# Kernel optimization log

Measured on AMD Instinct MI355X. Metric: run time of the kernel, lower is better.

## Reference

```python
import jax, jax.numpy as jnp
import numpy as np

NH, NL, NPNT = 8, 4, 4          # heads, levels, points
NQ, BS, NK, D, DFFN = 100, 8, 18, 256, 1024
SPATIAL = np.array([[92, 92], [46, 46], [23, 23], [12, 12]], np.int32)
LEN_MEM = int((SPATIAL[:, 0] * SPATIAL[:, 1]).sum())  # 11253


def _layernorm(x, g, b):
    m = x.mean(-1, keepdims=True)
    v = ((x - m) ** 2).mean(-1, keepdims=True)
    return (x - m) / jnp.sqrt(v + 1e-5) * g + b


def _mha(xq, xk, xv, in_w, in_b, out_w, out_b):
    # torch nn.MultiheadAttention semantics, inputs (S, B, D)
    S, B, d = xq.shape
    dh = d // NH
    wq, wk, wv = jnp.split(in_w, 3, axis=0)
    bq, bk, bv = jnp.split(in_b, 3, axis=0)
    def proj(x, w, b):
        return (x @ w.T + b).reshape(x.shape[0], B, NH, dh).transpose(1, 2, 0, 3)
    q = proj(xq, wq, bq) * (1.0 / np.sqrt(dh))
    k = proj(xk, wk, bk)
    v = proj(xv, wv, bv)
    att = jax.nn.softmax(jnp.einsum('bhqd,bhkd->bhqk', q, k), axis=-1)
    o = jnp.einsum('bhqk,bhkd->bhqd', att, v).transpose(2, 0, 1, 3).reshape(S, B, d)
    return o @ out_w.T + out_b


def _bilinear(v_l, loc):
    # v_l: (bs,H,W,NH,dh); loc: (bs,Lq,NH,P,2) normalized [0,1]
    # matches F.grid_sample(align_corners=False, padding_mode='zeros')
    bs, H, W, nh, dh = v_l.shape
    x = loc[..., 0] * W - 0.5
    y = loc[..., 1] * H - 0.5
    x0 = jnp.floor(x); y0 = jnp.floor(y)
    lx = x - x0; ly = y - y0
    b_idx = jnp.arange(bs)[:, None, None, None]
    h_idx = jnp.arange(nh)[None, None, :, None]
    def corner(xa, ya, w):
        valid = (xa >= 0) & (xa < W) & (ya >= 0) & (ya < H)
        xi = jnp.clip(xa, 0, W - 1).astype(jnp.int32)
        yi = jnp.clip(ya, 0, H - 1).astype(jnp.int32)
        return v_l[b_idx, yi, xi, h_idx] * (w * valid)[..., None]
    return (corner(x0, y0, (1 - lx) * (1 - ly)) + corner(x0 + 1, y0, lx * (1 - ly))
            + corner(x0, y0 + 1, (1 - lx) * ly) + corner(x0 + 1, y0 + 1, lx * ly))


def _msda(q, rp, mem, pad_mask, ss, off_w, off_b, aw_w, aw_b, val_w, val_b, outp_w, outp_b):
    bs, Lq, d = q.shape
    dh = d // NH
    value = mem @ val_w.T + val_b
    value = jnp.where(pad_mask[..., None], 0.0, value).reshape(bs, -1, NH, dh)
    off = (q @ off_w.T + off_b).reshape(bs, Lq, NH, NL, NPNT, 2)
    aw = jax.nn.softmax((q @ aw_w.T + aw_b).reshape(bs, Lq, NH, NL * NPNT), -1)
    aw = aw.reshape(bs, Lq, NH, NL, NPNT)
    wh = jnp.asarray(ss[:, ::-1].copy(), jnp.float32)  # offset normalizer (W, H)
    loc = rp[:, :, None, :, None, :] + off / wh[None, None, None, :, None, :]
    out = jnp.zeros((bs, Lq, NH, dh), q.dtype)
    start = 0
    for l in range(NL):
        H, W = int(ss[l, 0]), int(ss[l, 1])
        v_l = value[:, start:start + H * W].reshape(bs, H, W, NH, dh)
        start += H * W
        samp = _bilinear(v_l, loc[:, :, :, l])          # (bs,Lq,NH,P,dh)
        out = out + (samp * aw[:, :, :, l, :, None]).sum(3)
    return out.reshape(bs, Lq, d) @ outp_w.T + outp_b


def _forward(tgt_pose, pos, ref_points, memory, w_in_w, w_in_b, w_out_w, w_out_b,
             a_in_w, a_in_b, a_out_w, a_out_b, off_w, off_b, aw_w, aw_b,
             val_w, val_b, outp_w, outp_b, wn_g, wn_b, an_g, an_b,
             n1_g, n1_b, n2_g, n2_b, l1_w, l1_b, l2_w, l2_b,
             spatial_shapes, level_start_index, padding_mask):
    ss = np.asarray(jax.device_get(spatial_shapes))
    nq, bs, nk, d = tgt_pose.shape
    # within-group self-attn over the nk keypoint tokens.
    # NOTE: with_pos_embed mutates tgt_pose in place in the torch code, so
    # q = k = v = tgt + pos and the residual also uses tgt + pos (faithful).
    t = tgt_pose + pos
    x = t.reshape(nq * bs, nk, d).transpose(1, 0, 2)   # (nk, nq*bs, d)
    a1 = _mha(x, x, x, w_in_w, w_in_b, w_out_w, w_out_b)
    t = _layernorm(t + a1.transpose(1, 0, 2).reshape(nq, bs, nk, d), wn_g, wn_b)
    # across-group self-attn over the nq groups
    x2 = t.reshape(nq, bs * nk, d)
    a2 = _mha(x2, x2, x2, a_in_w, a_in_b, a_out_w, a_out_b)
    t = _layernorm(t + a2.reshape(nq, bs, nk, d), an_g, an_b)
    # MSDeformAttn cross-attention (in-place pos add again, faithful)
    t = t + pos
    q = t.transpose(1, 0, 2, 3).reshape(bs, nq * nk, d)
    rp = jnp.swapaxes(ref_points, 0, 1)                # (bs, nq*nk, NL, 2)
    mem = jnp.swapaxes(memory, 0, 1)                   # (bs, LEN_MEM, d)
    c = _msda(q, rp, mem, padding_mask, ss, off_w, off_b, aw_w, aw_b,
              val_w, val_b, outp_w, outp_b)
    c = c.reshape(bs, nq, nk, d).transpose(1, 0, 2, 3)
    t = _layernorm(t + c, n1_g, n1_b)
    # FFN (dropout is identity in eval)
    h = jax.nn.relu(t @ l1_w.T + l1_b)
    return _layernorm(t + (h @ l2_w.T + l2_b), n2_g, n2_b)


def setup_inputs() -> dict:
    key = jax.random.key(0)
    ks = jax.random.split(key, 16)
    p = lambda k, shape: jax.random.normal(k, shape, jnp.float32) * 0.02
    lsi = np.concatenate([[0], np.cumsum(SPATIAL[:, 0] * SPATIAL[:, 1])[:-1]]).astype(np.int32)
    return {
        'tgt_pose': jax.random.normal(ks[0], (NQ, BS, NK, D), jnp.float32),
        'pos': jax.random.normal(ks[1], (NQ, BS, NK, D), jnp.float32),
        'ref_points': jax.random.uniform(ks[2], (NQ * NK, BS, NL, 2), jnp.float32),
        'memory': jax.random.normal(ks[3], (LEN_MEM, BS, D), jnp.float32),
        'w_in_w': p(ks[4], (3 * D, D)), 'w_in_b': jnp.zeros((3 * D,)),
        'w_out_w': p(ks[5], (D, D)), 'w_out_b': jnp.zeros((D,)),
        'a_in_w': p(ks[6], (3 * D, D)), 'a_in_b': jnp.zeros((3 * D,)),
        'a_out_w': p(ks[7], (D, D)), 'a_out_b': jnp.zeros((D,)),
        'off_w': p(ks[8], (NH * NL * NPNT * 2, D)),
        'off_b': jax.random.uniform(ks[9], (NH * NL * NPNT * 2,), jnp.float32, -2.0, 2.0),
        'aw_w': p(ks[10], (NH * NL * NPNT, D)), 'aw_b': jnp.zeros((NH * NL * NPNT,)),
        'val_w': p(ks[11], (D, D)), 'val_b': jnp.zeros((D,)),
        'outp_w': p(ks[12], (D, D)), 'outp_b': jnp.zeros((D,)),
        'wn_g': jnp.ones((D,)), 'wn_b': jnp.zeros((D,)),
        'an_g': jnp.ones((D,)), 'an_b': jnp.zeros((D,)),
        'n1_g': jnp.ones((D,)), 'n1_b': jnp.zeros((D,)),
        'n2_g': jnp.ones((D,)), 'n2_b': jnp.zeros((D,)),
        'l1_w': p(ks[13], (DFFN, D)), 'l1_b': jnp.zeros((DFFN,)),
        'l2_w': p(ks[14], (D, DFFN)), 'l2_b': jnp.zeros((D,)),
        'spatial_shapes': jnp.asarray(SPATIAL),
        'level_start_index': jnp.asarray(lsi),
        'padding_mask': jnp.zeros((BS, LEN_MEM), bool),
    }


def reference(tgt_pose, pos, ref_points, memory, w_in_w, w_in_b, w_out_w, w_out_b,
              a_in_w, a_in_b, a_out_w, a_out_b, off_w, off_b, aw_w, aw_b,
              val_w, val_b, outp_w, outp_b, wn_g, wn_b, an_g, an_b,
              n1_g, n1_b, n2_g, n2_b, l1_w, l1_b, l2_w, l2_b,
              spatial_shapes, level_start_index, padding_mask):
    return _forward(tgt_pose, pos, ref_points, memory, w_in_w, w_in_b, w_out_w, w_out_b,
                    a_in_w, a_in_b, a_out_w, a_out_b, off_w, off_b, aw_w, aw_b,
                    val_w, val_b, outp_w, outp_b, wn_g, wn_b, an_g, an_b,
                    n1_g, n1_b, n2_g, n2_b, l1_w, l1_b, l2_w, l2_b,
                    spatial_shapes, level_start_index, padding_mask)
```

## Files before the change

kernel.cpp:

```cpp
#include <hip/hip_runtime.h>
#include <math.h>

#define NH_ 8
#define D_ 256
#define NK_ 18
#define NQ_ 100
#define BS_ 8
#define LQ_ 1800
#define LEN_MEM_ 11253
#define NTOK_ 14400

typedef short bf16x8 __attribute__((ext_vector_type(8)));
typedef float f32x4 __attribute__((ext_vector_type(4)));
typedef unsigned short ushort;

__device__ inline ushort f2bf(float f) {
    unsigned int u = __builtin_bit_cast(unsigned int, f);
    unsigned int r = (u + 0x7fffu + ((u >> 16) & 1u)) >> 16;
    return (ushort)r;
}
__device__ inline float bf2f_hi(unsigned int u) {
    unsigned int i = u & 0xffff0000u;
    return __builtin_bit_cast(float, i);
}
__device__ inline float bf2f_lo(unsigned int u) {
    unsigned int i = u << 16;
    return __builtin_bit_cast(float, i);
}
__device__ inline int packbf2(float a, float b) {
    return (int)f2bf(a) | ((int)f2bf(b) << 16);
}

__global__ __launch_bounds__(256)
void wcvt_kernel(const float* s0, const float* s1, const float* s2, const float* s3,
                 const float* s4, const float* s5, const float* s6, const float* s7,
                 const float* s8, const float* s9, ushort* dst) {
    const int sizes[10] = {196608,65536,196608,65536,65536,32768,65536,65536,262144,262144};
    const int offs[10]  = {0,196608,262144,458752,524288,589824,622592,688128,753664,1015808};
    int ti = blockIdx.y;
    const float* s;
    switch (ti) {
        case 0: s = s0; break; case 1: s = s1; break; case 2: s = s2; break;
        case 3: s = s3; break; case 4: s = s4; break; case 5: s = s5; break;
        case 6: s = s6; break; case 7: s = s7; break; case 8: s = s8; break;
        default: s = s9; break;
    }
    int n = sizes[ti];
    int i = (blockIdx.x * 256 + threadIdx.x) * 8;
    if (i >= n) return;
    ushort* d = dst + offs[ti] + i;
    float4 f0 = *(const float4*)(s + i);
    float4 f1 = *(const float4*)(s + i + 4);
    int4 val;
    val.x = packbf2(f0.x, f0.y);
    val.y = packbf2(f0.z, f0.w);
    val.z = packbf2(f1.x, f1.y);
    val.w = packbf2(f1.z, f1.w);
    *(int4*)d = val;
}

__global__ __launch_bounds__(256)
void addcvt_kernel(const float* __restrict__ a, const float* __restrict__ b,
                   float* __restrict__ c, ushort* __restrict__ cbf, int n4) {
    int i = blockIdx.x * blockDim.x + threadIdx.x;
    if (i >= n4) return;
    float4 av = ((const float4*)a)[i];
    float4 bv = ((const float4*)b)[i];
    float4 cv;
    cv.x = av.x + bv.x; cv.y = av.y + bv.y; cv.z = av.z + bv.z; cv.w = av.w + bv.w;
    ((float4*)c)[i] = cv;
    uint2 p;
    p.x = (unsigned int)packbf2(cv.x, cv.y);
    p.y = (unsigned int)packbf2(cv.z, cv.w);
    *(uint2*)(cbf + (size_t)i * 4) = p;
}

template<int MODE, bool RELU, bool A_F32, bool OUT_BF16, int BN, int WAVES, int R>
__device__ __forceinline__
void gemmw_body(int bx, int by, const void* __restrict__ Av, const ushort* __restrict__ W,
                const float* __restrict__ bias, void* __restrict__ Cv,
                int M, int N, const unsigned char* __restrict__ mask, ushort* Ws) {
    constexpr int K = 256;
    constexpr int NT = BN / 16;
    const int tid = threadIdx.x;
    const int m0 = bx * (WAVES * 16 * R);
    const int n0 = by * BN;

    for (int c = tid; c < 32 * BN; c += WAVES * 64) {
        int kc = c & 31, n = c >> 5;
        int dst = kc * BN + (n ^ (kc & 7));
        *(int4*)(Ws + dst * 8) = *(const int4*)(W + (long)(n0 + n) * K + kc * 8);
    }
    __syncthreads();

    const int wv = tid >> 6, lane = tid & 63, fr = lane & 15, hi = lane >> 4;
    const int wm0 = m0 + wv * (16 * R);
    long arow[R];
#pragma unroll
    for (int r = 0; r < R; ++r) {
        int gr = wm0 + r * 16 + fr;
        if (gr > M - 1) gr = M - 1;
        if (MODE == 2) {
            int b = gr / LQ_; int lq = gr - b * LQ_;
            int q = lq / NK_; int kk = lq - q * NK_;
            arow[r] = (long)q * (BS_ * NK_) + b * NK_ + kk;
        } else {
            arow[r] = gr;
        }
    }

    f32x4 acc[R][NT];
#pragma unroll
    for (int r = 0; r < R; ++r)
#pragma unroll
        for (int t = 0; t < NT; ++t) acc[r][t] = f32x4{0.f, 0.f, 0.f, 0.f};

    if (A_F32) {
        const float* ap[R];
        float4 p0[R], p1[R];
#pragma unroll
        for (int r = 0; r < R; ++r) {
            ap[r] = (const float*)Av + arow[r] * (long)K + hi * 8;
            p0[r] = *(const float4*)ap[r];
            p1[r] = *(const float4*)(ap[r] + 4);
        }
#pragma unroll
        for (int ks = 0; ks < 8; ++ks) {
            bf16x8 cur[R];
#pragma unroll
            for (int r = 0; r < R; ++r) {
                int4 v;
                v.x = packbf2(p0[r].x, p0[r].y); v.y = packbf2(p0[r].z, p0[r].w);
                v.z = packbf2(p1[r].x, p1[r].y); v.w = packbf2(p1[r].z, p1[r].w);
                cur[r] = __builtin_bit_cast(bf16x8, v);
                if (ks < 7) {
                    p0[r] = *(const float4*)(ap[r] + (ks + 1) * 32);
                    p1[r] = *(const float4*)(ap[r] + (ks + 1) * 32 + 4);
                }
            }
            const int kc = ks * 4 + hi;
            const ushort* wb = Ws + ((kc * BN) + (fr ^ (kc & 7))) * 8;
#pragma unroll
            for (int t = 0; t < NT; ++t) {
                bf16x8 wf = *(const bf16x8*)(wb + t * 128);
#pragma unroll
                for (int r = 0; r < R; ++r)
                    acc[r][t] = __builtin_amdgcn_mfma_f32_16x16x32_bf16(cur[r], wf, acc[r][t], 0, 0, 0);
            }
        }
    } else {
        const ushort* ap[R];
        bf16x8 afrag[R];
#pragma unroll
        for (int r = 0; r < R; ++r) {
            ap[r] = (const ushort*)Av + arow[r] * (long)K + hi * 8;
            afrag[r] = *(const bf16x8*)ap[r];
        }
#pragma unroll
        for (int ks = 0; ks < 8; ++ks) {
            bf16x8 cur[R];
#pragma unroll
            for (int r = 0; r < R; ++r) {
                cur[r] = afrag[r];
                if (ks < 7) afrag[r] = *(const bf16x8*)(ap[r] + (ks + 1) * 32);
            }
            const int kc = ks * 4 + hi;
            const ushort* wb = Ws + ((kc * BN) + (fr ^ (kc & 7))) * 8;
#pragma unroll
            for (int t = 0; t < NT; ++t) {
                bf16x8 wf = *(const bf16x8*)(wb + t * 128);
#pragma unroll
                for (int r = 0; r < R; ++r)
                    acc[r][t] = __builtin_amdgcn_mfma_f32_16x16x32_bf16(cur[r], wf, acc[r][t], 0, 0, 0);
            }
        }
    }

#pragma unroll
    for (int r = 0; r < R; ++r) {
#pragma unroll
        for (int rr = 0; rr < 4; ++rr) {
            int gm = wm0 + r * 16 + hi * 4 + rr;
            if (gm >= M) continue;
            long orow = gm;
            bool zero = false;
            if (MODE == 1) {
                if (mask && mask[(size_t)(gm & 7) * LEN_MEM_ + (gm >> 3)]) zero = true;
            } else if (MODE == 3) {
                int b = gm / LQ_; int lq = gm - b * LQ_;
                int q = lq / NK_; int kk = lq - q * NK_;
                orow = (long)q * (BS_ * NK_) + b * NK_ + kk;
            }
#pragma unroll
            for (int t = 0; t < NT; ++t) {
                int gn = n0 + t * 16 + fr;
                float v = acc[r][t][rr] + bias[gn];
                if (RELU) v = fmaxf(v, 0.f);
                if (zero) v = 0.f;
                if (OUT_BF16) ((ushort*)Cv)[orow * (long)N + gn] = f2bf(v);
                else ((float*)Cv)[orow * (long)N + gn] = v;
            }
        }
    }
}

template<int MODE, bool RELU, bool A_F32, bool OUT_BF16, int BN, int WAVES, int R>
__global__ __launch_bounds__(WAVES * 64)
void gemmw_kernel(const void* __restrict__ Av, const ushort* __restrict__ W,
                  const float* __restrict__ bias, void* __restrict__ Cv,
                  int M, int N, const unsigned char* __restrict__ mask) {
    __shared__ ushort Ws[32 * BN * 8];
    gemmw_body<MODE, RELU, A_F32, OUT_BF16, BN, WAVES, R>(
        blockIdx.x, blockIdx.y, Av, W, bias, Cv, M, N, mask, Ws);
}

__global__ __launch_bounds__(512)
void fusedqv_kernel(const float* __restrict__ memA, const ushort* __restrict__ Wv,
                    const float* __restrict__ bv, ushort* __restrict__ Cval,
                    const unsigned char* __restrict__ mask,
                    const ushort* __restrict__ Aq, const ushort* __restrict__ Wq,
                    const float* __restrict__ bq, ushort* __restrict__ Cq) {
    __shared__ ushort Ws[32 * 128 * 8];
    int idx = blockIdx.x;
    int g3 = idx / 3, r3 = idx - g3 * 3;
    if (r3 < 2) {
        int v = g3 * 2 + r3;
        gemmw_body<1, false, true, true, 128, 8, 2>(v >> 1, v & 1, memA, Wv, bv, Cval,
                                                    90024, 256, mask, Ws);
    } else {
        int q = g3;
        if (q < 342)
            gemmw_body<0, false, false, true, 128, 8, 2>(q % 57, q / 57, Aq, Wq, bq, Cq,
                                                         NTOK_, 768, nullptr, Ws);
    }
}

__global__ __launch_bounds__(256)
void fusedoa_kernel(const ushort* __restrict__ A,
                    const ushort* __restrict__ Woff, const float* __restrict__ boff, float* __restrict__ Coff,
                    const ushort* __restrict__ Waw, const float* __restrict__ baw, float* __restrict__ Caw) {
    __shared__ ushort Ws[32 * 64 * 8];
    int by = blockIdx.y;
    if (by < 4)
        gemmw_body<2, false, false, false, 64, 4, 2>(blockIdx.x, by, A, Woff, boff, Coff, NTOK_, 256, nullptr, Ws);
    else
        gemmw_body<2, false, false, false, 64, 4, 2>(blockIdx.x, by - 4, A, Waw, baw, Caw, NTOK_, 128, nullptr, Ws);
}

template<int MODE, bool RELU, bool A_F32, bool OUT_BF16>
__global__ __launch_bounds__(256)
void gemm_kernel(const void* __restrict__ Av, const ushort* __restrict__ W,
                 const float* __restrict__ bias, void* __restrict__ Cv,
                 int M, int N, int K, const unsigned char* __restrict__ mask) {
    constexpr int AST = 72;
    __shared__ ushort As[128 * AST];
    __shared__ ushort Bs[128 * AST];
    const int m0 = blockIdx.x * 128, n0 = blockIdx.y * 128;
    const int tid = threadIdx.x;
    const int w = tid >> 6, lane = tid & 63;
    const int wr = w >> 1, wc = w & 1;
    const int fr = lane & 15, hi = lane >> 4;
    f32x4 acc[4][4];
#pragma unroll
    for (int i = 0; i < 4; ++i)
#pragma unroll
        for (int j = 0; j < 4; ++j) acc[i][j] = f32x4{0.f, 0.f, 0.f, 0.f};

    const int srow = tid >> 1, shalf = tid & 1;
    long arow = 0;
    const bool avalid = (m0 + srow) < M;
    {
        int gr = m0 + srow;
        if (gr >= M) gr = M - 1;
        arow = gr;
    }

    for (int k0 = 0; k0 < K; k0 += 64) {
        ushort* ad = As + srow * AST + shalf * 32;
        if (avalid) {
            const ushort* ap = (const ushort*)Av + arow * (long)K + k0 + shalf * 32;
#pragma unroll
            for (int i = 0; i < 4; ++i) *(int4*)(ad + i * 8) = *(const int4*)(ap + i * 8);
        } else {
            int4 z = make_int4(0, 0, 0, 0);
#pragma unroll
            for (int i = 0; i < 4; ++i) *(int4*)(ad + i * 8) = z;
        }
        {
            const ushort* wp = W + (long)(n0 + srow) * K + k0 + shalf * 32;
            ushort* bd = Bs + srow * AST + shalf * 32;
#pragma unroll
            for (int i = 0; i < 4; ++i) *(int4*)(bd + i * 8) = *(const int4*)(wp + i * 8);
        }
        __syncthreads();
#pragma unroll
        for (int kb = 0; kb < 2; ++kb) {
            bf16x8 af[4], bfr[4];
#pragma unroll
            for (int i = 0; i < 4; ++i)
                af[i] = *(const bf16x8*)(As + (wr * 64 + i * 16 + fr) * AST + kb * 32 + hi * 8);
#pragma unroll
            for (int j = 0; j < 4; ++j)
                bfr[j] = *(const bf16x8*)(Bs + (wc * 64 + j * 16 + fr) * AST + kb * 32 + hi * 8);
#pragma unroll
            for (int i = 0; i < 4; ++i)
#pragma unroll
                for (int j = 0; j < 4; ++j)
                    acc[i][j] = __builtin_amdgcn_mfma_f32_16x16x32_bf16(af[i], bfr[j], acc[i][j], 0, 0, 0);
        }
        __syncthreads();
    }

#pragma unroll
    for (int i = 0; i < 4; ++i) {
#pragma unroll
        for (int r = 0; r < 4; ++r) {
            int gm = m0 + wr * 64 + i * 16 + hi * 4 + r;
            if (gm >= M) continue;
#pragma unroll
            for (int j = 0; j < 4; ++j) {
                int gn = n0 + wc * 64 + j * 16 + fr;
                float v = acc[i][j][r] + bias[gn];
                if (RELU) v = fmaxf(v, 0.f);
                if (OUT_BF16) ((ushort*)Cv)[(long)gm * N + gn] = f2bf(v);
                else ((float*)Cv)[(long)gm * N + gn] = v;
            }
        }
    }
}

template<int S, int SP, int HPB>
__global__ __launch_bounds__(256)
void mattn_kernel(const ushort* __restrict__ qkv, ushort* __restrict__ outb,
                  int rsG, int rsS) {
    constexpr int SPk = ((SP + 31) / 32) * 32;
    constexpr int KST = 40;
    constexpr int PST = SPk + 8;
    constexpr int NT = SP / 16;
    constexpr int NB = HPB * NT;
    constexpr int HB = 8 / HPB;
    __shared__ ushort KsA[HPB * SP * KST];
    __shared__ ushort VtA[HPB * 32 * PST];
    __shared__ ushort PA [HPB * SP * PST];

    const int tid = threadIdx.x;
    const int g = blockIdx.x / HB;
    const int hbase = (blockIdx.x % HB) * HPB;

    for (int idx = tid; idx < HPB * S * 4; idx += 256) {
        int hh = idx / (S * 4); int rem = idx - hh * (S * 4);
        int j = rem >> 2, q = rem & 3;
        const ushort* base = qkv + ((size_t)g * rsG + (size_t)j * rsS) * 768 + (hbase + hh) * 32 + q * 8;
        uint4 kv = *(const uint4*)(base + 256);
        ushort* kd = KsA + hh * (SP * KST) + j * KST + q * 8;
        *(uint2*)kd = make_uint2(kv.x, kv.y);
        *(uint2*)(kd + 4) = make_uint2(kv.z, kv.w);
        uint4 vv = *(const uint4*)(base + 512);
        ushort* vt = VtA + hh * (32 * PST) + j;
        unsigned int uu[4] = {vv.x, vv.y, vv.z, vv.w};
#pragma unroll
        for (int e = 0; e < 4; ++e) {
            vt[(q * 8 + e * 2    ) * PST] = (ushort)(uu[e] & 0xffff);
            vt[(q * 8 + e * 2 + 1) * PST] = (ushort)(uu[e] >> 16);
        }
    }
    for (int idx = tid; idx < HPB * 32 * (SPk - S); idx += 256) {
        int hh = idx / (32 * (SPk - S)); int rem = idx - hh * (32 * (SPk - S));
        int d = rem / (SPk - S); int c = S + rem - d * (SPk - S);
        VtA[hh * 32 * PST + d * PST + c] = 0;
    }
    if constexpr (SPk > SP) {
        constexpr int PW = SPk - SP;
        for (int idx = tid; idx < HPB * SP * PW; idx += 256) {
            int hh = idx / (SP * PW); int rem = idx - hh * (SP * PW);
            int rrow = rem / PW; int c = SP + rem - rrow * PW;
            PA[hh * SP * PST + rrow * PST + c] = 0;
        }
    }
    __syncthreads();

    const int wv = tid >> 6, lane = tid & 63, fr = lane & 15, hi = lane >> 4;
    for (int band = wv; band < NB; band += 4) {
        const int hh = band / NT, mb = band - (band / NT) * NT;
        const int h = hbase + hh;
        const ushort* Ks = KsA + hh * (SP * KST);
        const ushort* Vt = VtA + hh * (32 * PST);
        ushort* P = PA + hh * (SP * PST);

        int sq = mb * 16 + fr; if (sq > S - 1) sq = S - 1;
        bf16x8 qf = *(const bf16x8*)(qkv + ((size_t)g * rsG + (size_t)sq * rsS) * 768 + h * 32 + hi * 8);
        f32x4 sc[NT];
#pragma unroll
        for (int t = 0; t < NT; ++t) {
            bf16x8 kf = *(const bf16x8*)(Ks + (t * 16 + fr) * KST + hi * 8);
            sc[t] = __builtin_amdgcn_mfma_f32_16x16x32_bf16(qf, kf, f32x4{0.f, 0.f, 0.f, 0.f}, 0, 0, 0);
        }
#pragma unroll
        for (int t = 0; t < NT; ++t) {
            bool valid = (t * 16 + fr) < S;
#pragma unroll
            for (int r = 0; r < 4; ++r)
                sc[t][r] = valid ? sc[t][r] * 0.17677669529663687f : -1e30f;
        }
#pragma unroll
        for (int r = 0; r < 4; ++r) {
            float m = sc[0][r];
#pragma unroll
            for (int t = 1; t < NT; ++t) m = fmaxf(m, sc[t][r]);
            m = fmaxf(m, __shfl_xor(m, 1)); m = fmaxf(m, __shfl_xor(m, 2));
            m = fmaxf(m, __shfl_xor(m, 4)); m = fmaxf(m, __shfl_xor(m, 8));
            float e[NT]; float sum = 0.f;
#pragma unroll
            for (int t = 0; t < NT; ++t) { e[t] = __expf(sc[t][r] - m); sum += e[t]; }
            sum += __shfl_xor(sum, 1); sum += __shfl_xor(sum, 2);
            sum += __shfl_xor(sum, 4); sum += __shfl_xor(sum, 8);
            float inv = 1.f / sum;
            int row = mb * 16 + hi * 4 + r;
#pragma unroll
            for (int t = 0; t < NT; ++t)
                P[row * PST + t * 16 + fr] = f2bf(e[t] * inv);
        }
        f32x4 o0 = {0.f, 0.f, 0.f, 0.f}, o1 = {0.f, 0.f, 0.f, 0.f};
#pragma unroll
        for (int kb = 0; kb < SPk / 32; ++kb) {
            bf16x8 pf = *(const bf16x8*)(P + (mb * 16 + fr) * PST + kb * 32 + hi * 8);
            bf16x8 v0 = *(const bf16x8*)(Vt + fr * PST + kb * 32 + hi * 8);
            bf16x8 v1 = *(const bf16x8*)(Vt + (16 + fr) * PST + kb * 32 + hi * 8);
            o0 = __builtin_amdgcn_mfma_f32_16x16x32_bf16(pf, v0, o0, 0, 0, 0);
            o1 = __builtin_amdgcn_mfma_f32_16x16x32_bf16(pf, v1, o1, 0, 0, 0);
        }
#pragma unroll
        for (int r = 0; r < 4; ++r) {
            int s = mb * 16 + hi * 4 + r;
            if (s < S) {
                size_t ob = ((size_t)g * rsG + (size_t)s * rsS) * 256 + h * 32;
                outb[ob + fr] = f2bf(o0[r]);
                outb[ob + 16 + fr] = f2bf(o1[r]);
            }
        }
    }
}

__global__ __launch_bounds__(256)
void addln_kernel(const float* __restrict__ base, const ushort* __restrict__ delta,
                  const float* __restrict__ gamma, const float* __restrict__ beta,
                  const float* __restrict__ pos,
                  float* __restrict__ out, ushort* __restrict__ obf, int M) {
    int row = blockIdx.x * 4 + (threadIdx.x >> 6);
    int lane = threadIdx.x & 63;
    if (row >= M) return;
    const size_t rb = (size_t)row * 256 + lane * 4;
    float4 bv = *(const float4*)(base + rb);
    uint2 du = *(const uint2*)(delta + rb);
    float v[4];
    v[0] = bv.x + bf2f_lo(du.x);
    v[1] = bv.y + bf2f_hi(du.x);
    v[2] = bv.z + bf2f_lo(du.y);
    v[3] = bv.w + bf2f_hi(du.y);
    float s = v[0] + v[1] + v[2] + v[3];
#pragma unroll
    for (int off = 32; off; off >>= 1) s += __shfl_xor(s, off);
    float mean = s * (1.f / 256.f);
    float var = 0.f;
#pragma unroll
    for (int i = 0; i < 4; ++i) { float d = v[i] - mean; var += d * d; }
#pragma unroll
    for (int off = 32; off; off >>= 1) var += __shfl_xor(var, off);
    var *= (1.f / 256.f);
    float rstd = rsqrtf(var + 1e-5f);
    float4 gv = *(const float4*)(gamma + lane * 4);
    float4 bev = *(const float4*)(beta + lane * 4);
    float o[4];
    o[0] = (v[0] - mean) * rstd * gv.x + bev.x;
    o[1] = (v[1] - mean) * rstd * gv.y + bev.y;
    o[2] = (v[2] - mean) * rstd * gv.z + bev.z;
    o[3] = (v[3] - mean) * rstd * gv.w + bev.w;
    if (pos) {
        float4 pv = *(const float4*)(pos + rb);
        o[0] += pv.x; o[1] += pv.y; o[2] += pv.z; o[3] += pv.w;
    }
    float4 ov; ov.x = o[0]; ov.y = o[1]; ov.z = o[2]; ov.w = o[3];
    *(float4*)(out + rb) = ov;
    if (obf) {
        uint2 p;
        p.x = (unsigned int)packbf2(o[0], o[1]);
        p.y = (unsigned int)packbf2(o[2], o[3]);
        *(uint2*)(obf + rb) = p;
    }
}

__global__ __launch_bounds__(256)
void msda_kernel(const float* __restrict__ offb, const float* __restrict__ aw,
                 const ushort* __restrict__ val, const float* __restrict__ refp,
                 const int* __restrict__ spatial, const int* __restrict__ lsi,
                 ushort* __restrict__ samp) {
    const int unit = blockIdx.x * 32 + (threadIdx.x >> 3);
    const int lane8 = threadIdx.x & 7;
    const int base8 = (threadIdx.x & 63) & 56;
    const int h = unit & 7;
    const int t = unit >> 3;
    const int lq = t % LQ_;
    const int b = t / LQ_;
    const size_t row = (size_t)b * LQ_ + lq;

    float2 lg = *(const float2*)(aw + row * 128 + h * 16 + lane8 * 2);
    float m = fmaxf(lg.x, lg.y);
    m = fmaxf(m, __shfl_xor(m, 1)); m = fmaxf(m, __shfl_xor(m, 2)); m = fmaxf(m, __shfl_xor(m, 4));
    float e0 = __expf(lg.x - m), e1 = __expf(lg.y - m);
    float s = e0 + e1;
    s += __shfl_xor(s, 1); s += __shfl_xor(s, 2); s += __shfl_xor(s, 4);
    float inv = 1.f / s;
    float w0 = e0 * inv, w1 = e1 * inv;

    float4 of = *(const float4*)(offb + row * 256 + h * 32 + lane8 * 4);

    const float* rp = refp + ((size_t)lq * BS_ + b) * 8;
    float4 rp0 = *(const float4*)rp;
    float4 rp1 = *(const float4*)(rp + 4);

    float acc[4] = {0.f, 0.f, 0.f, 0.f};

#pragma unroll 1
    for (int lvl = 0; lvl < 4; ++lvl) {
        int H = spatial[lvl * 2], W = spatial[lvl * 2 + 1];
        int st = lsi[lvl];
        float rpx = (lvl == 0) ? rp0.x : (lvl == 1) ? rp0.z : (lvl == 2) ? rp1.x : rp1.z;
        float rpy = (lvl == 0) ? rp0.y : (lvl == 1) ? rp0.w : (lvl == 2) ? rp1.y : rp1.w;
        const ushort* vb = val + ((size_t)st * 8 + b) * 256 + h * 32 + lane8 * 4;
        float fW = (float)W, fH = (float)H;
#pragma unroll
        for (int p = 0; p < 4; ++p) {
            float ox_ = (p & 1) ? of.z : of.x;
            float oy_ = (p & 1) ? of.w : of.y;
            float wp_ = (p & 1) ? w1 : w0;
            int src = base8 + lvl * 2 + (p >> 1);
            float ox  = __shfl(ox_, src);
            float oy  = __shfl(oy_, src);
            float wpt = __shfl(wp_, src);

            float x = rpx * fW + ox - 0.5f;
            float y = rpy * fH + oy - 0.5f;
            float x0f = floorf(x), y0f = floorf(y);
            float lx = x - x0f, ly = y - y0f;
            int x0 = (int)x0f, y0 = (int)y0f;
            int xc0 = min(max(x0, 0), W - 1), xc1 = min(max(x0 + 1, 0), W - 1);
            int yc0 = min(max(y0, 0), H - 1), yc1 = min(max(y0 + 1, 0), H - 1);
            float vx0 = (x0 >= 0 && x0 < W) ? 1.f : 0.f;
            float vx1 = (x0 >= -1 && x0 + 1 < W) ? 1.f : 0.f;
            float vy0 = (y0 >= 0 && y0 < H) ? 1.f : 0.f;
            float vy1 = (y0 >= -1 && y0 + 1 < H) ? 1.f : 0.f;
            float w00 = wpt * (1.f - lx) * (1.f - ly) * vx0 * vy0;
            float w10 = wpt * lx * (1.f - ly) * vx1 * vy0;
            float w01 = wpt * (1.f - lx) * ly * vx0 * vy1;
            float w11 = wpt * lx * ly * vx1 * vy1;
            uint2 u00 = *(const uint2*)(vb + (size_t)(yc0 * W + xc0) * 2048);
            uint2 u10 = *(const uint2*)(vb + (size_t)(yc0 * W + xc1) * 2048);
            uint2 u01 = *(const uint2*)(vb + (size_t)(yc1 * W + xc0) * 2048);
            uint2 u11 = *(const uint2*)(vb + (size_t)(yc1 * W + xc1) * 2048);
            acc[0] += w00 * bf2f_lo(u00.x) + w10 * bf2f_lo(u10.x)
                    + w01 * bf2f_lo(u01.x) + w11 * bf2f_lo(u11.x);
            acc[1] += w00 * bf2f_hi(u00.x) + w10 * bf2f_hi(u10.x)
                    + w01 * bf2f_hi(u01.x) + w11 * bf2f_hi(u11.x);
            acc[2] += w00 * bf2f_lo(u00.y) + w10 * bf2f_lo(u10.y)
                    + w01 * bf2f_lo(u01.y) + w11 * bf2f_lo(u11.y);
            acc[3] += w00 * bf2f_hi(u00.y) + w10 * bf2f_hi(u10.y)
                    + w01 * bf2f_hi(u01.y) + w11 * bf2f_hi(u11.y);
        }
    }
    size_t o = row * 256 + h * 32 + lane8 * 4;
    uint2 pk;
    pk.x = (unsigned int)packbf2(acc[0], acc[1]);
    pk.y = (unsigned int)packbf2(acc[2], acc[3]);
    *(uint2*)(samp + o) = pk;
}

extern "C" void kernel_launch(void* const* d_in, const int* in_sizes, int n_in,
                              void* d_out, int out_size, void* d_ws, size_t ws_size,
                              hipStream_t stream) {
    const float* tgt     = (const float*)d_in[0];
    const float* pos     = (const float*)d_in[1];
    const float* refp    = (const float*)d_in[2];
    const float* memory  = (const float*)d_in[3];
    const float* w_in_w  = (const float*)d_in[4];
    const float* w_in_b  = (const float*)d_in[5];
    const float* w_out_w = (const float*)d_in[6];
    const float* w_out_b = (const float*)d_in[7];
    const float* a_in_w  = (const float*)d_in[8];
    const float* a_in_b  = (const float*)d_in[9];
    const float* a_out_w = (const float*)d_in[10];
    const float* a_out_b = (const float*)d_in[11];
    const float* off_w   = (const float*)d_in[12];
    const float* off_b   = (const float*)d_in[13];
    const float* aw_w    = (const float*)d_in[14];
    const float* aw_b    = (const float*)d_in[15];
    const float* val_w   = (const float*)d_in[16];
    const float* val_b   = (const float*)d_in[17];
    const float* outp_w  = (const float*)d_in[18];
    const float* outp_b  = (const float*)d_in[19];
    const float* wn_g    = (const float*)d_in[20];
    const float* wn_b    = (const float*)d_in[21];
    const float* an_g    = (const float*)d_in[22];
    const float* an_b    = (const float*)d_in[23];
    const float* n1_g    = (const float*)d_in[24];
    const float* n1_b    = (const float*)d_in[25];
    const float* n2_g    = (const float*)d_in[26];
    const float* n2_b    = (const float*)d_in[27];
    const float* l1_w    = (const float*)d_in[28];
    const float* l1_b    = (const float*)d_in[29];
    const float* l2_w    = (const float*)d_in[30];
    const float* l2_b    = (const float*)d_in[31];
    const int*   spatial = (const int*)d_in[32];
    const int*   lsi     = (const int*)d_in[33];
    const unsigned char* pmask = (const unsigned char*)d_in[34];
    float* out = (float*)d_out;

    float*  T      = (float*)d_ws;
    ushort* Tbf    = (ushort*)(T + 3686400);
    ushort* B16    = Tbf + 3686400;
    ushort* CBbf   = B16 + 11059200;
    ushort* VALbf  = CBbf + 3686400;
    ushort* SAMPbf = VALbf + 23046144;
    ushort* Hbf    = SAMPbf + 3686400;
    ushort* WB     = Hbf + 14745600;
    float*  OFF    = (float*)(WB + 1277952);
    float*  AW     = OFF + 3686400;
    ushort* OFFbf  = (ushort*)(AW + 1843200);

    ushort* WB_win  = WB + 0;
    ushort* WB_wout = WB + 196608;
    ushort* WB_ain  = WB + 262144;
    ushort* WB_aout = WB + 458752;
    ushort* WB_off  = WB + 524288;
    ushort* WB_aw   = WB + 589824;
    ushort* WB_val  = WB + 622592;
    ushort* WB_outp = WB + 688128;
    ushort* WB_l1   = WB + 753664;
    ushort* WB_l2   = WB + 1015808;

    const int n4 = NTOK_ * 256 / 4;

    wcvt_kernel<<<dim3(128, 10), 256, 0, stream>>>(
        w_in_w, w_out_w, a_in_w, a_out_w, off_w, aw_w, val_w, outp_w, l1_w, l2_w, WB);
    addcvt_kernel<<<n4 / 256, 256, 0, stream>>>(tgt, pos, T, Tbf, n4);
    fusedqv_kernel<<<3 * 352, 512, 0, stream>>>(
        memory, WB_val, val_b, VALbf, pmask, Tbf, WB_win, w_in_b, B16);
    mattn_kernel<18, 32, 4><<<800 * 2, 256, 0, stream>>>(B16, CBbf, 18, 1);
    gemmw_kernel<0, false, false, true, 64, 4, 2><<<dim3(113, 4), 256, 0, stream>>>(
        CBbf, WB_wout, w_out_b, OFFbf, NTOK_, 256, nullptr);
    addln_kernel<<<NTOK_ / 4, 256, 0, stream>>>(T, OFFbf, wn_g, wn_b, nullptr, T, Tbf, NTOK_);
    gemmw_kernel<0, false, false, true, 64, 4, 2><<<dim3(113, 12), 256, 0, stream>>>(
        Tbf, WB_ain, a_in_b, B16, NTOK_, 768, nullptr);
    mattn_kernel<100, 112, 1><<<144 * 8, 256, 0, stream>>>(B16, CBbf, 1, 144);
    gemmw_kernel<0, false, false, true, 64, 4, 2><<<dim3(113, 4), 256, 0, stream>>>(
        CBbf, WB_aout, a_out_b, OFFbf, NTOK_, 256, nullptr);
    addln_kernel<<<NTOK_ / 4, 256, 0, stream>>>(T, OFFbf, an_g, an_b, pos, T, Tbf, NTOK_);
    fusedoa_kernel<<<dim3(113, 6), 256, 0, stream>>>(
        Tbf, WB_off, off_b, OFF, WB_aw, aw_b, AW);
    msda_kernel<<<3600, 256, 0, stream>>>(OFF, AW, VALbf, refp, spatial, lsi, SAMPbf);
    gemmw_kernel<3, false, false, true, 64, 4, 2><<<dim3(113, 4), 256, 0, stream>>>(
        SAMPbf, WB_outp, outp_b, OFFbf, NTOK_, 256, nullptr);
    addln_kernel<<<NTOK_ / 4, 256, 0, stream>>>(T, OFFbf, n1_g, n1_b, nullptr, T, Tbf, NTOK_);
    gemmw_kernel<0, true, false, true, 64, 4, 2><<<dim3(113, 16), 256, 0, stream>>>(
        Tbf, WB_l1, l1_b, Hbf, NTOK_, 1024, nullptr);
    gemm_kernel<0, false, false, true><<<dim3(113, 2), 256, 0, stream>>>(
        Hbf, WB_l2, l2_b, OFFbf, NTOK_, 256, 1024, nullptr);
    addln_kernel<<<NTOK_ / 4, 256, 0, stream>>>(T, OFFbf, n2_g, n2_b, nullptr, out, nullptr, NTOK_);
}
```

Measured before the change: 321.2 us.

## Split value projection across two fused launches and widen attention block to seven waves

```diff
diff --git a/kernel.cpp b/kernel.cpp
--- a/kernel.cpp
+++ b/kernel.cpp
@@ -217,18 +217,17 @@
 __global__ __launch_bounds__(512)
 void fusedqv_kernel(const float* __restrict__ memA, const ushort* __restrict__ Wv,
                     const float* __restrict__ bv, ushort* __restrict__ Cval,
-                    const unsigned char* __restrict__ mask,
+                    const unsigned char* __restrict__ mask, int voff,
                     const ushort* __restrict__ Aq, const ushort* __restrict__ Wq,
                     const float* __restrict__ bq, ushort* __restrict__ Cq) {
     __shared__ ushort Ws[32 * 128 * 8];
     int idx = blockIdx.x;
-    int g3 = idx / 3, r3 = idx - g3 * 3;
-    if (r3 < 2) {
-        int v = g3 * 2 + r3;
+    if ((idx & 1) == 0) {
+        int v = voff + (idx >> 1);
         gemmw_body<1, false, true, true, 128, 8, 2>(v >> 1, v & 1, memA, Wv, bv, Cval,
                                                     90024, 256, mask, Ws);
     } else {
-        int q = g3;
+        int q = idx >> 1;
         if (q < 342)
             gemmw_body<0, false, false, true, 128, 8, 2>(q % 57, q / 57, Aq, Wq, bq, Cq,
                                                          NTOK_, 768, nullptr, Ws);
@@ -329,10 +328,11 @@
     }
 }
 
-template<int S, int SP, int HPB>
-__global__ __launch_bounds__(256)
+template<int S, int SP, int HPB, int WAVES>
+__global__ __launch_bounds__(WAVES * 64)
 void mattn_kernel(const ushort* __restrict__ qkv, ushort* __restrict__ outb,
                   int rsG, int rsS) {
+    constexpr int NTH = WAVES * 64;
     constexpr int SPk = ((SP + 31) / 32) * 32;
     constexpr int KST = 40;
     constexpr int PST = SPk + 8;
@@ -347,7 +347,7 @@
     const int g = blockIdx.x / HB;
     const int hbase = (blockIdx.x % HB) * HPB;
 
-    for (int idx = tid; idx < HPB * S * 4; idx += 256) {
+    for (int idx = tid; idx < HPB * S * 4; idx += NTH) {
         int hh = idx / (S * 4); int rem = idx - hh * (S * 4);
         int j = rem >> 2, q = rem & 3;
         const ushort* base = qkv + ((size_t)g * rsG + (size_t)j * rsS) * 768 + (hbase + hh) * 32 + q * 8;
@@ -364,14 +364,14 @@
             vt[(q * 8 + e * 2 + 1) * PST] = (ushort)(uu[e] >> 16);
         }
     }
-    for (int idx = tid; idx < HPB * 32 * (SPk - S); idx += 256) {
+    for (int idx = tid; idx < HPB * 32 * (SPk - S); idx += NTH) {
         int hh = idx / (32 * (SPk - S)); int rem = idx - hh * (32 * (SPk - S));
         int d = rem / (SPk - S); int c = S + rem - d * (SPk - S);
         VtA[hh * 32 * PST + d * PST + c] = 0;
     }
     if constexpr (SPk > SP) {
         constexpr int PW = SPk - SP;
-        for (int idx = tid; idx < HPB * SP * PW; idx += 256) {
+        for (int idx = tid; idx < HPB * SP * PW; idx += NTH) {
             int hh = idx / (SP * PW); int rem = idx - hh * (SP * PW);
             int rrow = rem / PW; int c = SP + rem - rrow * PW;
             PA[hh * SP * PST + rrow * PST + c] = 0;
@@ -380,7 +380,7 @@
     __syncthreads();
 
     const int wv = tid >> 6, lane = tid & 63, fr = lane & 15, hi = lane >> 4;
-    for (int band = wv; band < NB; band += 4) {
+    for (int band = wv; band < NB; band += WAVES) {
         const int hh = band / NT, mb = band - (band / NT) * NT;
         const int h = hbase + hh;
         const ushort* Ks = KsA + hh * (SP * KST);
@@ -642,15 +642,15 @@
     wcvt_kernel<<<dim3(128, 10), 256, 0, stream>>>(
         w_in_w, w_out_w, a_in_w, a_out_w, off_w, aw_w, val_w, outp_w, l1_w, l2_w, WB);
     addcvt_kernel<<<n4 / 256, 256, 0, stream>>>(tgt, pos, T, Tbf, n4);
-    fusedqv_kernel<<<3 * 352, 512, 0, stream>>>(
-        memory, WB_val, val_b, VALbf, pmask, Tbf, WB_win, w_in_b, B16);
-    mattn_kernel<18, 32, 4><<<800 * 2, 256, 0, stream>>>(B16, CBbf, 18, 1);
+    fusedqv_kernel<<<704, 512, 0, stream>>>(
+        memory, WB_val, val_b, VALbf, pmask, 0, Tbf, WB_win, w_in_b, B16);
+    mattn_kernel<18, 32, 4, 4><<<800 * 2, 256, 0, stream>>>(B16, CBbf, 18, 1);
     gemmw_kernel<0, false, false, true, 64, 4, 2><<<dim3(113, 4), 256, 0, stream>>>(
         CBbf, WB_wout, w_out_b, OFFbf, NTOK_, 256, nullptr);
     addln_kernel<<<NTOK_ / 4, 256, 0, stream>>>(T, OFFbf, wn_g, wn_b, nullptr, T, Tbf, NTOK_);
-    gemmw_kernel<0, false, false, true, 64, 4, 2><<<dim3(113, 12), 256, 0, stream>>>(
-        Tbf, WB_ain, a_in_b, B16, NTOK_, 768, nullptr);
-    mattn_kernel<100, 112, 1><<<144 * 8, 256, 0, stream>>>(B16, CBbf, 1, 144);
+    fusedqv_kernel<<<704, 512, 0, stream>>>(
+        memory, WB_val, val_b, VALbf, pmask, 352, Tbf, WB_ain, a_in_b, B16);
+    mattn_kernel<100, 112, 1, 7><<<144 * 8, 448, 0, stream>>>(B16, CBbf, 1, 144);
     gemmw_kernel<0, false, false, true, 64, 4, 2><<<dim3(113, 4), 256, 0, stream>>>(
         CBbf, WB_aout, a_out_b, OFFbf, NTOK_, 256, nullptr);
     addln_kernel<<<NTOK_ / 4, 256, 0, stream>>>(T, OFFbf, an_g, an_b, pos, T, Tbf, NTOK_);
```

Result: no change. 324.2 us (+0.9%).
